# Kernel tuning notes

Hardware: AMD Instinct MI355X
Metric: run time of the kernel (lower is better)

Reference implementation:

```python
import jax, jax.numpy as jnp
import numpy as np
import math

C_S, C_Z, H, D, P_QK, P_V = 384, 128, 12, 16, 4, 8
B, L = 1, 512

def setup_inputs() -> dict:
    ks = jax.random.split(jax.random.key(0), 16)
    sc = lambda fan_in: 1.0 / math.sqrt(fan_in)
    return {
        's': jax.random.normal(ks[0], (B, L, C_S), jnp.float32),
        'z': jax.random.normal(ks[1], (B, L, L, C_Z), jnp.float32),
        'R': jax.random.normal(ks[2], (B, L, 3, 3), jnp.float32),
        't': jax.random.normal(ks[3], (B, L, 3), jnp.float32),
        'g_s': jnp.ones((C_S,), jnp.float32),
        'b_s': jnp.zeros((C_S,), jnp.float32),
        'g_z': jnp.ones((C_Z,), jnp.float32),
        'b_z': jnp.zeros((C_Z,), jnp.float32),
        'Wq': jax.random.normal(ks[4], (C_S, H * D), jnp.float32) * sc(C_S),
        'Wk': jax.random.normal(ks[5], (C_S, H * D), jnp.float32) * sc(C_S),
        'Wv': jax.random.normal(ks[6], (C_S, H * D), jnp.float32) * sc(C_S),
        'Wqp': jax.random.normal(ks[7], (C_S, H * P_QK * 3), jnp.float32) * sc(C_S),
        'Wkp': jax.random.normal(ks[8], (C_S, H * P_QK * 3), jnp.float32) * sc(C_S),
        'Wvp': jax.random.normal(ks[9], (C_S, H * P_V * 3), jnp.float32) * sc(C_S),
        'Wpb': jax.random.normal(ks[10], (C_Z, H), jnp.float32) * sc(C_Z),
        'pw': jax.random.normal(ks[11], (H,), jnp.float32) * 0.1,
        'Wo': jax.random.normal(ks[12], (H * D + H * P_V * 3 + H * P_V, C_S), jnp.float32) * sc(H * D + H * P_V * 3 + H * P_V),
        'bo': jnp.zeros((C_S,), jnp.float32),
    }

def _ln(x, g, b, eps=1e-5):
    mu = jnp.mean(x, axis=-1, keepdims=True)
    var = jnp.mean(jnp.square(x - mu), axis=-1, keepdims=True)
    return (x - mu) * jax.lax.rsqrt(var + eps) * g + b

def reference(s, z, R, t, g_s, b_s, g_z, b_z, Wq, Wk, Wv, Wqp, Wkp, Wvp, Wpb, pw, Wo, bo):
    Bn, Ln, _ = s.shape
    sn = _ln(s, g_s, b_s)
    zn = _ln(z, g_z, b_z)
    q_s = (sn @ Wq).reshape(Bn, Ln, H, D)
    k_s = (sn @ Wk).reshape(Bn, Ln, H, D)
    v_s = (sn @ Wv).reshape(Bn, Ln, H, D)
    q_pl = (sn @ Wqp).reshape(Bn, Ln, H, P_QK, 3)
    k_pl = (sn @ Wkp).reshape(Bn, Ln, H, P_QK, 3)
    v_pl = (sn @ Wvp).reshape(Bn, Ln, H, P_V, 3)
    # local->global frame transform: x_global = R x_local + t
    tb = t[:, :, None, None, :]
    q_p = jnp.einsum('blij,blhpj->blhpi', R, q_pl) + tb
    k_p = jnp.einsum('blij,blhpj->blhpi', R, k_pl) + tb
    v_p = jnp.einsum('blij,blhpj->blhpi', R, v_pl) + tb
    scalar_logits = jnp.einsum('bihd,bjhd->bijh', q_s, k_s) / math.sqrt(D)
    pair_logits = zn @ Wpb  # (B,L,L,H)
    # sum_p |q_ip - k_jp|^2 without materializing the (B,L,L,H,P,3) diff tensor
    qn2 = jnp.sum(jnp.square(q_p), axis=(-1, -2))  # (B,L,H)
    kn2 = jnp.sum(jnp.square(k_p), axis=(-1, -2))
    qk = jnp.einsum('bihpc,bjhpc->bijh', q_p, k_p)
    dist2 = qn2[:, :, None, :] + kn2[:, None, :, :] - 2.0 * qk
    w = jax.nn.softplus(pw)[None, None, None, :]
    logits = scalar_logits + pair_logits - 0.5 * w * dist2
    attn = jax.nn.softmax(logits, axis=2)  # over keys j
    out_s = jnp.einsum('bijh,bjhd->bihd', attn, v_s)
    out_pg = jnp.einsum('bijh,bjhpc->bihpc', attn, v_p)
    # global->local: R^T (x - t); (R^T)_{xy} = R_{yx}
    out_pl = jnp.einsum('blyx,blhpy->blhpx', R, out_pg - tb)
    out_pn = jnp.sqrt(jnp.sum(jnp.square(out_pl), axis=-1) + 1e-8)
    out_cat = jnp.concatenate([out_s.reshape(Bn, Ln, -1), out_pl.reshape(Bn, Ln, -1), out_pn.reshape(Bn, Ln, -1)], axis=-1)
    return s + out_cat @ Wo + bo
```

## Files before the change

### kernel.cpp

```cpp
#include <hip/hip_runtime.h>

typedef float f32x4 __attribute__((ext_vector_type(4)));
typedef short bf16x8 __attribute__((ext_vector_type(8)));

#define MFMA16(a,b,c) __builtin_amdgcn_mfma_f32_16x16x32_bf16((a),(b),(c),0,0,0)

__device__ __forceinline__ unsigned short f2bf(float f){
  unsigned int u = __builtin_bit_cast(unsigned int, f);
  u += 0x7FFFu + ((u>>16)&1u);
  return (unsigned short)(u>>16);
}

#define OFF_SNBF  0u
#define OFF_PROJ  393216u
#define OFF_QP    2752512u
#define OFF_KFRAG 3047424u
#define OFF_VFRAG 3440640u
#define OFF_KN2   4030464u
#define OFF_PLT   4055040u
#define OFF_OBUF  16637952u
#define OFF_CATBF 17620992u
#define OFF_WPBF  18210816u
#define OFF_GZF   18214912u
#define OFF_BZF   18223104u
#define OFF_WCF   18231296u
#define OFF_WOF   19116032u
#define OFF_WBUF  19558400u

__global__ __launch_bounds__(256) void k_prep(
    const float* __restrict__ Wq, const float* __restrict__ Wk, const float* __restrict__ Wv,
    const float* __restrict__ Wqp, const float* __restrict__ Wkp, const float* __restrict__ Wvp,
    const float* __restrict__ Wpb, const float* __restrict__ pw, const float* __restrict__ Wo,
    const float* __restrict__ g_z, const float* __restrict__ b_z,
    unsigned short* __restrict__ wpbfrag, float* __restrict__ gzfrag, float* __restrict__ bzfrag,
    unsigned short* __restrict__ wcfrag, unsigned short* __restrict__ wofrag,
    float* __restrict__ wbuf){
  int idx = blockIdx.x*256 + threadIdx.x;
  const int N_wpb = 2048, N_gz = 2048, N_wc = 72*12*64*8, N_wo = 24*18*64*8;
  if (idx < N_wpb){
    int r = idx&7, lane=(idx>>3)&63, chunk=idx>>9;
    int c = chunk*32 + ((lane>>4)<<3) + r; int h = lane&15;
    wpbfrag[idx] = (h<12) ? f2bf(Wpb[c*12+h]) : (unsigned short)0;
    return;
  }
  idx -= N_wpb;
  if (idx < N_gz){
    int r = idx&7, lane=(idx>>3)&63, chunk=idx>>9;
    int c = chunk*32 + ((lane>>4)<<3) + r;
    gzfrag[idx] = g_z[c]; bzfrag[idx] = b_z[c];
    return;
  }
  idx -= N_gz;
  if (idx < N_wc){
    int r = idx&7, lane=(idx>>3)&63, kt=(idx>>9)%12, nt=idx/(12*512);
    int k = kt*32 + ((lane>>4)<<3) + r; int n = nt*16 + (lane&15);
    float v;
    if      (n < 192) v = Wq [k*192 + n];
    else if (n < 384) v = Wk [k*192 + (n-192)];
    else if (n < 576) v = Wv [k*192 + (n-384)];
    else if (n < 720) v = Wqp[k*144 + (n-576)];
    else if (n < 864) v = Wkp[k*144 + (n-720)];
    else              v = Wvp[k*288 + (n-864)];
    wcfrag[idx] = f2bf(v);
    return;
  }
  idx -= N_wc;
  if (idx < N_wo){
    int r = idx&7, lane=(idx>>3)&63, kt=(idx>>9)%18, nt=idx/(18*512);
    int k = kt*32 + ((lane>>4)<<3) + r; int n = nt*16 + (lane&15);
    wofrag[idx] = f2bf(Wo[k*384 + n]);
    return;
  }
  idx -= N_wo;
  if (idx < 12){
    float x = pw[idx];
    wbuf[idx] = log1pf(expf(x));
  }
}

__global__ __launch_bounds__(64) void k_lns(const float* __restrict__ s,
    const float* __restrict__ g_s, const float* __restrict__ b_s,
    unsigned short* __restrict__ snbf){
  int l = blockIdx.x; int lane = threadIdx.x;
  float v[6]; float sum=0.f, ss=0.f;
  #pragma unroll
  for (int k=0;k<6;k++){
    float x = s[l*384 + lane + 64*k];
    v[k]=x; sum += x; ss = fmaf(x,x,ss);
  }
  #pragma unroll
  for (int m=1;m<64;m<<=1){ sum += __shfl_xor(sum,m); ss += __shfl_xor(ss,m); }
  float mu = sum*(1.f/384.f);
  float var = ss*(1.f/384.f) - mu*mu;
  float rs = rsqrtf(var + 1e-5f);
  #pragma unroll
  for (int k=0;k<6;k++){
    int c = lane + 64*k;
    snbf[l*384 + c] = f2bf((v[k]-mu)*rs*g_s[c] + b_s[c]);
  }
}

__global__ __launch_bounds__(256) void k_proj(const unsigned short* __restrict__ snbf,
    const unsigned short* __restrict__ wcfrag, float* __restrict__ proj){
  int wid = blockIdx.x*4 + (threadIdx.x>>6);
  int lane = threadIdx.x & 63;
  int il = lane&15, ig = lane>>4;
  int nt = wid % 72, ib = wid / 72;
  int i0 = ib*16;
  f32x4 acc = {0.f,0.f,0.f,0.f};
  #pragma unroll
  for (int kt=0; kt<12; kt++){
    bf16x8 a = *(const bf16x8*)(snbf + (i0+il)*384 + kt*32 + ig*8);
    bf16x8 b = *(const bf16x8*)(wcfrag + (size_t)((nt*12+kt)*64 + lane)*8);
    acc = MFMA16(a, b, acc);
  }
  #pragma unroll
  for (int r=0;r<4;r++)
    proj[(i0 + ig*4 + r)*1152 + nt*16 + il] = acc[r];
}

__global__ __launch_bounds__(192) void k_points(const float* __restrict__ proj,
    const float* __restrict__ Rm, const float* __restrict__ tv,
    float* __restrict__ qpb, unsigned short* __restrict__ kfrag,
    unsigned short* __restrict__ vfrag, float* __restrict__ kn2T){
  int l = blockIdx.x; int t = threadIdx.x;
  __shared__ float Rl[9], tl[3];
  __shared__ float kp_lds[12][12];
  __shared__ float vp_lds[12][24];
  __shared__ float kn2acc[12][4];
  if (t < 9) Rl[t] = Rm[l*9 + t];
  if (t < 3) tl[t] = tv[l*3 + t];
  __syncthreads();
  int h = t >> 4, pt = t & 15;
  {
    int ptype = (pt<4)? 0 : ((pt<8)? 1 : 2);
    int p = pt - ((ptype==0)?0:((ptype==1)?4:8));
    int col0 = (ptype==0)?576:((ptype==1)?720:864);
    int stride = (ptype==2)?24:12;
    const float* src = proj + l*1152 + col0 + h*stride + p*3;
    float lx=src[0], ly=src[1], lz=src[2];
    float cx = Rl[0]*lx + Rl[1]*ly + Rl[2]*lz + tl[0];
    float cy = Rl[3]*lx + Rl[4]*ly + Rl[5]*lz + tl[1];
    float cz = Rl[6]*lx + Rl[7]*ly + Rl[8]*lz + tl[2];
    if (ptype==0){
      float* d = qpb + (l*12 + h)*12 + p*3;
      d[0]=cx; d[1]=cy; d[2]=cz;
    } else if (ptype==1){
      kp_lds[h][p*3+0]=cx; kp_lds[h][p*3+1]=cy; kp_lds[h][p*3+2]=cz;
      kn2acc[h][p] = cx*cx + cy*cy + cz*cz;
    } else {
      vp_lds[h][p*3+0]=cx; vp_lds[h][p*3+1]=cy; vp_lds[h][p*3+2]=cz;
    }
  }
  __syncthreads();
  if (t < 12)
    kn2T[t*512 + l] = kn2acc[t][0]+kn2acc[t][1]+kn2acc[t][2]+kn2acc[t][3];
  {
    int jt = l >> 4, jl = l & 15;
    int q = pt >> 2, rr = (pt & 3)*2;
    unsigned short* dst = kfrag + (size_t)((h*32 + jt)*64 + 16*q + jl)*8 + rr;
    #pragma unroll
    for (int e=0;e<2;e++){
      int k = pt*2 + e; float f;
      if (k < 16)      f = proj[l*1152 + 192 + h*16 + k];
      else if (k < 28) f = kp_lds[h][k-16];
      else             f = 0.f;
      dst[e] = f2bf(f);
    }
  }
  {
    int d = pt; int jc = l >> 5; int jin = l & 31;
    int qq = (jin & 15) >> 2;
    int rr = (jin & 3) + ((jin >> 4) << 2);
    #pragma unroll
    for (int dt=0; dt<3; dt++){
      int dd = dt*16 + d; float f;
      if (dd < 16)      f = proj[l*1152 + 384 + h*16 + dd];
      else if (dd < 40) f = vp_lds[h][dd-16];
      else              f = 0.f;
      vfrag[(size_t)(((h*16 + jc)*3 + dt)*64 + 16*qq + d)*8 + rr] = f2bf(f);
    }
  }
}

__global__ __launch_bounds__(256) void k_pairbias(const float* __restrict__ z,
    const unsigned short* __restrict__ wpbfrag, const float* __restrict__ gzfrag,
    const float* __restrict__ bzfrag, const float* __restrict__ kn2T,
    const float* __restrict__ wbuf, float* __restrict__ plT){
  int w = blockIdx.x*4 + (threadIdx.x>>6);
  int lane = threadIdx.x & 63;
  int il = lane & 15, ig = lane >> 4;
  int nw = gridDim.x*4;
  f32x4 gzv[8], bzv[8];
  bf16x8 wf[4];
  #pragma unroll
  for (int c=0;c<4;c++){
    gzv[2*c]   = *(const f32x4*)(gzfrag + (c*64+lane)*8);
    gzv[2*c+1] = *(const f32x4*)(gzfrag + (c*64+lane)*8 + 4);
    bzv[2*c]   = *(const f32x4*)(bzfrag + (c*64+lane)*8);
    bzv[2*c+1] = *(const f32x4*)(bzfrag + (c*64+lane)*8 + 4);
    wf[c] = *(const bf16x8*)(wpbfrag + (c*64+lane)*8);
  }
  float wneg = (il<12) ? -0.5f*wbuf[il] : 0.f;
  for (int g = w; g < 16384; g += nw){
    int j = g >> 5; int i0 = (g & 31) << 4;
    const float* zr = z + (size_t)((i0+il)*512 + j)*128;
    f32x4 zv[8];
    #pragma unroll
    for (int c=0;c<4;c++){
      zv[2*c]   = *(const f32x4*)(zr + c*32 + ig*8);
      zv[2*c+1] = *(const f32x4*)(zr + c*32 + ig*8 + 4);
    }
    float sum=0.f, ss=0.f;
    #pragma unroll
    for (int m=0;m<8;m++)
      #pragma unroll
      for (int e=0;e<4;e++){ float x = zv[m][e]; sum += x; ss = fmaf(x,x,ss); }
    sum += __shfl_xor(sum,16); sum += __shfl_xor(sum,32);
    ss  += __shfl_xor(ss,16);  ss  += __shfl_xor(ss,32);
    float mu  = sum*(1.f/128.f);
    float var = ss*(1.f/128.f) - mu*mu;
    float rs  = rsqrtf(var + 1e-5f);
    f32x4 acc = {0.f,0.f,0.f,0.f};
    #pragma unroll
    for (int c=0;c<4;c++){
      bf16x8 zf;
      #pragma unroll
      for (int r=0;r<8;r++){
        float gv = (r<4)? gzv[2*c][r&3] : gzv[2*c+1][r&3];
        float bv = (r<4)? bzv[2*c][r&3] : bzv[2*c+1][r&3];
        float xv = (r<4)? zv[2*c][r&3]  : zv[2*c+1][r&3];
        zf[r] = (short)f2bf((xv-mu)*(rs*gv) + bv);
      }
      acc = MFMA16(zf, wf[c], acc);
    }
    if (il < 12){
      float tadd = wneg * kn2T[il*512 + j];
      f32x4 ov;
      ov[0]=acc[0]+tadd; ov[1]=acc[1]+tadd; ov[2]=acc[2]+tadd; ov[3]=acc[3]+tadd;
      *(f32x4*)(plT + (size_t)(il*512 + j)*512 + i0 + ig*4) = ov;
    }
  }
}

__global__ __launch_bounds__(64) void k_attn(const float* __restrict__ proj,
    const float* __restrict__ qpb, const float* __restrict__ wbuf,
    const unsigned short* __restrict__ kfrag, const float* __restrict__ plT,
    const unsigned short* __restrict__ vfrag, float* __restrict__ obuf){
  int u = blockIdx.x;
  int h = u % 12, ib = u / 12;
  int i0 = ib*16;
  int lane = threadIdx.x;
  int il = lane & 15, ig = lane >> 4;
  float wh = wbuf[h];
  bf16x8 qfrag;
  #pragma unroll
  for (int r=0;r<8;r++){
    int k = ig*8 + r; float f;
    if (k < 16)      f = proj[(i0+il)*1152 + h*16 + k]*0.25f;
    else if (k < 28) f = qpb[((i0+il)*12 + h)*12 + (k-16)]*wh;
    else             f = 0.f;
    qfrag[r] = (short)f2bf(f);
  }
  f32x4 sv[32];
  const unsigned short* kbase = kfrag + (size_t)(h*32)*64*8;
  #pragma unroll
  for (int jt=0;jt<32;jt++){
    bf16x8 kf = *(const bf16x8*)(kbase + (size_t)(jt*64 + lane)*8);
    f32x4 c0;
    #pragma unroll
    for (int r=0;r<4;r++)
      c0[r] = plT[(size_t)(h*512 + jt*16 + ig*4 + r)*512 + i0 + il];
    sv[jt] = MFMA16(kf, qfrag, c0);
  }
  float mx = -3.0e38f;
  #pragma unroll
  for (int jt=0;jt<32;jt++){
    #pragma unroll
    for (int r=0;r<4;r++) mx = fmaxf(mx, sv[jt][r]);
  }
  mx = fmaxf(mx, __shfl_xor(mx,16));
  mx = fmaxf(mx, __shfl_xor(mx,32));
  float sum = 0.f;
  #pragma unroll
  for (int jt=0;jt<32;jt++){
    #pragma unroll
    for (int r=0;r<4;r++){ float p = __expf(sv[jt][r]-mx); sv[jt][r]=p; sum+=p; }
  }
  sum += __shfl_xor(sum,16);
  sum += __shfl_xor(sum,32);
  float rden = 1.f/sum;
  f32x4 o0={0.f,0.f,0.f,0.f}, o1=o0, o2=o0;
  const unsigned short* vbase = vfrag + (size_t)(h*16)*3*64*8;
  #pragma unroll
  for (int jc=0;jc<16;jc++){
    bf16x8 pfrag;
    #pragma unroll
    for (int r=0;r<8;r++) pfrag[r] = (short)f2bf(sv[2*jc + (r>>2)][r&3]);
    bf16x8 v0 = *(const bf16x8*)(vbase + (size_t)((jc*3+0)*64 + lane)*8);
    bf16x8 v1 = *(const bf16x8*)(vbase + (size_t)((jc*3+1)*64 + lane)*8);
    bf16x8 v2 = *(const bf16x8*)(vbase + (size_t)((jc*3+2)*64 + lane)*8);
    o0 = MFMA16(v0, pfrag, o0);
    o1 = MFMA16(v1, pfrag, o1);
    o2 = MFMA16(v2, pfrag, o2);
  }
  float* orow = obuf + (i0+il)*480 + h*40;
  #pragma unroll
  for (int r=0;r<4;r++){
    orow[ig*4 + r]      = o0[r]*rden;
    orow[16 + ig*4 + r] = o1[r]*rden;
    if (ig < 2) orow[32 + ig*4 + r] = o2[r]*rden;
  }
}

__global__ __launch_bounds__(192) void k_cat(const float* __restrict__ obuf,
    const float* __restrict__ Rm, const float* __restrict__ tv,
    unsigned short* __restrict__ catbf){
  int l = blockIdx.x; int t = threadIdx.x;
  __shared__ float Rl[9], tl[3];
  if (t < 9) Rl[t] = Rm[l*9 + t];
  if (t < 3) tl[t] = tv[l*3 + t];
  __syncthreads();
  catbf[l*576 + t] = f2bf(obuf[l*480 + (t>>4)*40 + (t&15)]);
  if (t < 96){
    int hh = t >> 3, p = t & 7;
    float oy0 = obuf[l*480 + hh*40 + 16 + p*3 + 0] - tl[0];
    float oy1 = obuf[l*480 + hh*40 + 16 + p*3 + 1] - tl[1];
    float oy2 = obuf[l*480 + hh*40 + 16 + p*3 + 2] - tl[2];
    float px = Rl[0]*oy0 + Rl[3]*oy1 + Rl[6]*oy2;
    float py = Rl[1]*oy0 + Rl[4]*oy1 + Rl[7]*oy2;
    float pz = Rl[2]*oy0 + Rl[5]*oy1 + Rl[8]*oy2;
    catbf[l*576 + 192 + t*3 + 0] = f2bf(px);
    catbf[l*576 + 192 + t*3 + 1] = f2bf(py);
    catbf[l*576 + 192 + t*3 + 2] = f2bf(pz);
    catbf[l*576 + 480 + t] = f2bf(sqrtf(px*px + py*py + pz*pz + 1e-8f));
  }
}

__global__ __launch_bounds__(256) void k_outgemm(const unsigned short* __restrict__ catbf,
    const unsigned short* __restrict__ wofrag, const float* __restrict__ s,
    const float* __restrict__ bo, float* __restrict__ out){
  int wid = blockIdx.x*4 + (threadIdx.x>>6);
  int lane = threadIdx.x & 63;
  int il = lane&15, ig = lane>>4;
  int nt = wid % 24, ib = wid / 24;
  int i0 = ib*16;
  int n = nt*16 + il;
  f32x4 acc = {0.f,0.f,0.f,0.f};
  #pragma unroll
  for (int kt=0; kt<18; kt++){
    bf16x8 a = *(const bf16x8*)(catbf + (i0+il)*576 + kt*32 + ig*8);
    bf16x8 b = *(const bf16x8*)(wofrag + (size_t)((nt*18+kt)*64 + lane)*8);
    acc = MFMA16(a, b, acc);
  }
  float bv = bo[n];
  #pragma unroll
  for (int r=0;r<4;r++){
    int row = i0 + ig*4 + r;
    out[row*384 + n] = s[row*384 + n] + bv + acc[r];
  }
}

extern "C" void kernel_launch(void* const* d_in, const int* in_sizes, int n_in,
                              void* d_out, int out_size, void* d_ws, size_t ws_size,
                              hipStream_t stream) {
  const float* s   = (const float*)d_in[0];
  const float* z   = (const float*)d_in[1];
  const float* R   = (const float*)d_in[2];
  const float* t   = (const float*)d_in[3];
  const float* g_s = (const float*)d_in[4];
  const float* b_s = (const float*)d_in[5];
  const float* g_z = (const float*)d_in[6];
  const float* b_z = (const float*)d_in[7];
  const float* Wq  = (const float*)d_in[8];
  const float* Wk  = (const float*)d_in[9];
  const float* Wv  = (const float*)d_in[10];
  const float* Wqp = (const float*)d_in[11];
  const float* Wkp = (const float*)d_in[12];
  const float* Wvp = (const float*)d_in[13];
  const float* Wpb = (const float*)d_in[14];
  const float* pw  = (const float*)d_in[15];
  const float* Wo  = (const float*)d_in[16];
  const float* bo  = (const float*)d_in[17];
  float* out = (float*)d_out;
  char* ws = (char*)d_ws;

  unsigned short* snbf    = (unsigned short*)(ws + OFF_SNBF);
  float*          proj    = (float*)(ws + OFF_PROJ);
  float*          qpb     = (float*)(ws + OFF_QP);
  unsigned short* kfrag   = (unsigned short*)(ws + OFF_KFRAG);
  unsigned short* vfrag   = (unsigned short*)(ws + OFF_VFRAG);
  float*          kn2T    = (float*)(ws + OFF_KN2);
  float*          plT     = (float*)(ws + OFF_PLT);
  float*          obuf    = (float*)(ws + OFF_OBUF);
  unsigned short* catbf   = (unsigned short*)(ws + OFF_CATBF);
  unsigned short* wpbfrag = (unsigned short*)(ws + OFF_WPBF);
  float*          gzfrag  = (float*)(ws + OFF_GZF);
  float*          bzfrag  = (float*)(ws + OFF_BZF);
  unsigned short* wcfrag  = (unsigned short*)(ws + OFF_WCF);
  unsigned short* wofrag  = (unsigned short*)(ws + OFF_WOF);
  float*          wbuf    = (float*)(ws + OFF_WBUF);

  k_prep<<<2609, 256, 0, stream>>>(Wq, Wk, Wv, Wqp, Wkp, Wvp, Wpb, pw, Wo, g_z, b_z,
                                   wpbfrag, gzfrag, bzfrag, wcfrag, wofrag, wbuf);
  k_lns<<<512, 64, 0, stream>>>(s, g_s, b_s, snbf);
  k_proj<<<576, 256, 0, stream>>>(snbf, wcfrag, proj);
  k_points<<<512, 192, 0, stream>>>(proj, R, t, qpb, kfrag, vfrag, kn2T);
  k_pairbias<<<1024, 256, 0, stream>>>(z, wpbfrag, gzfrag, bzfrag, kn2T, wbuf, plT);
  k_attn<<<384, 64, 0, stream>>>(proj, qpb, wbuf, kfrag, plT, vfrag, obuf);
  k_cat<<<512, 192, 0, stream>>>(obuf, R, t, catbf);
  k_outgemm<<<192, 256, 0, stream>>>(catbf, wofrag, s, bo, out);
}
```

Measured before the change: 71.17 us.

## Store pair bias in bf16, split attention keys across 8 waves, fold LN into prep

The pair-bias intermediate is now written as bf16 instead of fp32, which halves its write and read traffic. The kn2 distance term moves out of k_pairbias and into the attention kernel. k_attn now runs 512 threads per block, with each of 8 waves handling 64 keys and combining its softmax max, sum and output partials through LDS. The LayerNorm of s is merged into the prep kernel to save one launch. In exchange the pair logits lose precision, and the attention kernel gains barriers and LDS reductions.

```diff
diff --git a/kernel.cpp b/kernel.cpp
--- a/kernel.cpp
+++ b/kernel.cpp
@@ -2,6 +2,7 @@
 
 typedef float f32x4 __attribute__((ext_vector_type(4)));
 typedef short bf16x8 __attribute__((ext_vector_type(8)));
+typedef unsigned short u16x4 __attribute__((ext_vector_type(4)));
 
 #define MFMA16(a,b,c) __builtin_amdgcn_mfma_f32_16x16x32_bf16((a),(b),(c),0,0,0)
 
@@ -9,6 +10,9 @@
   unsigned int u = __builtin_bit_cast(unsigned int, f);
   u += 0x7FFFu + ((u>>16)&1u);
   return (unsigned short)(u>>16);
+}
+__device__ __forceinline__ float bf2f(unsigned short u){
+  return __builtin_bit_cast(float, ((unsigned int)u)<<16);
 }
 
 #define OFF_SNBF  0u
@@ -18,16 +22,18 @@
 #define OFF_VFRAG 3440640u
 #define OFF_KN2   4030464u
 #define OFF_PLT   4055040u
-#define OFF_OBUF  16637952u
-#define OFF_CATBF 17620992u
-#define OFF_WPBF  18210816u
-#define OFF_GZF   18214912u
-#define OFF_BZF   18223104u
-#define OFF_WCF   18231296u
-#define OFF_WOF   19116032u
-#define OFF_WBUF  19558400u
+#define OFF_OBUF  10346496u
+#define OFF_CATBF 11329536u
+#define OFF_WPBF  11919360u
+#define OFF_GZF   11923456u
+#define OFF_BZF   11931648u
+#define OFF_WCF   11939840u
+#define OFF_WOF   12824576u
+#define OFF_WBUF  13266944u
 
 __global__ __launch_bounds__(256) void k_prep(
+    const float* __restrict__ s, const float* __restrict__ g_s, const float* __restrict__ b_s,
+    unsigned short* __restrict__ snbf,
     const float* __restrict__ Wq, const float* __restrict__ Wk, const float* __restrict__ Wv,
     const float* __restrict__ Wqp, const float* __restrict__ Wkp, const float* __restrict__ Wvp,
     const float* __restrict__ Wpb, const float* __restrict__ pw, const float* __restrict__ Wo,
@@ -35,7 +41,28 @@
     unsigned short* __restrict__ wpbfrag, float* __restrict__ gzfrag, float* __restrict__ bzfrag,
     unsigned short* __restrict__ wcfrag, unsigned short* __restrict__ wofrag,
     float* __restrict__ wbuf){
-  int idx = blockIdx.x*256 + threadIdx.x;
+  if (blockIdx.x < 128){
+    int l = blockIdx.x*4 + (threadIdx.x>>6);
+    int lane = threadIdx.x & 63;
+    float v[6]; float sum=0.f, ss=0.f;
+    #pragma unroll
+    for (int k=0;k<6;k++){
+      float x = s[l*384 + lane + 64*k];
+      v[k]=x; sum += x; ss = fmaf(x,x,ss);
+    }
+    #pragma unroll
+    for (int m=1;m<64;m<<=1){ sum += __shfl_xor(sum,m); ss += __shfl_xor(ss,m); }
+    float mu = sum*(1.f/384.f);
+    float var = ss*(1.f/384.f) - mu*mu;
+    float rs = rsqrtf(var + 1e-5f);
+    #pragma unroll
+    for (int k=0;k<6;k++){
+      int c = lane + 64*k;
+      snbf[l*384 + c] = f2bf((v[k]-mu)*rs*g_s[c] + b_s[c]);
+    }
+    return;
+  }
+  int idx = (blockIdx.x-128)*256 + threadIdx.x;
   const int N_wpb = 2048, N_gz = 2048, N_wc = 72*12*64*8, N_wo = 24*18*64*8;
   if (idx < N_wpb){
     int r = idx&7, lane=(idx>>3)&63, chunk=idx>>9;
@@ -75,28 +102,6 @@
   if (idx < 12){
     float x = pw[idx];
     wbuf[idx] = log1pf(expf(x));
-  }
-}
-
-__global__ __launch_bounds__(64) void k_lns(const float* __restrict__ s,
-    const float* __restrict__ g_s, const float* __restrict__ b_s,
-    unsigned short* __restrict__ snbf){
-  int l = blockIdx.x; int lane = threadIdx.x;
-  float v[6]; float sum=0.f, ss=0.f;
-  #pragma unroll
-  for (int k=0;k<6;k++){
-    float x = s[l*384 + lane + 64*k];
-    v[k]=x; sum += x; ss = fmaf(x,x,ss);
-  }
-  #pragma unroll
-  for (int m=1;m<64;m<<=1){ sum += __shfl_xor(sum,m); ss += __shfl_xor(ss,m); }
-  float mu = sum*(1.f/384.f);
-  float var = ss*(1.f/384.f) - mu*mu;
-  float rs = rsqrtf(var + 1e-5f);
-  #pragma unroll
-  for (int k=0;k<6;k++){
-    int c = lane + 64*k;
-    snbf[l*384 + c] = f2bf((v[k]-mu)*rs*g_s[c] + b_s[c]);
   }
 }
 
@@ -185,8 +190,7 @@
 
 __global__ __launch_bounds__(256) void k_pairbias(const float* __restrict__ z,
     const unsigned short* __restrict__ wpbfrag, const float* __restrict__ gzfrag,
-    const float* __restrict__ bzfrag, const float* __restrict__ kn2T,
-    const float* __restrict__ wbuf, float* __restrict__ plT){
+    const float* __restrict__ bzfrag, unsigned short* __restrict__ plTbf){
   int w = blockIdx.x*4 + (threadIdx.x>>6);
   int lane = threadIdx.x & 63;
   int il = lane & 15, ig = lane >> 4;
@@ -201,7 +205,6 @@
     bzv[2*c+1] = *(const f32x4*)(bzfrag + (c*64+lane)*8 + 4);
     wf[c] = *(const bf16x8*)(wpbfrag + (c*64+lane)*8);
   }
-  float wneg = (il<12) ? -0.5f*wbuf[il] : 0.f;
   for (int g = w; g < 16384; g += nw){
     int j = g >> 5; int i0 = (g & 31) << 4;
     const float* zr = z + (size_t)((i0+il)*512 + j)*128;
@@ -235,24 +238,30 @@
       acc = MFMA16(zf, wf[c], acc);
     }
     if (il < 12){
-      float tadd = wneg * kn2T[il*512 + j];
-      f32x4 ov;
-      ov[0]=acc[0]+tadd; ov[1]=acc[1]+tadd; ov[2]=acc[2]+tadd; ov[3]=acc[3]+tadd;
-      *(f32x4*)(plT + (size_t)(il*512 + j)*512 + i0 + ig*4) = ov;
-    }
-  }
-}
-
-__global__ __launch_bounds__(64) void k_attn(const float* __restrict__ proj,
+      u16x4 ov;
+      #pragma unroll
+      for (int r=0;r<4;r++) ov[r] = f2bf(acc[r]);
+      *(u16x4*)(plTbf + (size_t)(il*512 + j)*512 + i0 + ig*4) = ov;
+    }
+  }
+}
+
+__global__ __launch_bounds__(512) void k_attn(const float* __restrict__ proj,
     const float* __restrict__ qpb, const float* __restrict__ wbuf,
-    const unsigned short* __restrict__ kfrag, const float* __restrict__ plT,
-    const unsigned short* __restrict__ vfrag, float* __restrict__ obuf){
+    const unsigned short* __restrict__ kfrag, const unsigned short* __restrict__ plTbf,
+    const float* __restrict__ kn2T, const unsigned short* __restrict__ vfrag,
+    float* __restrict__ obuf){
   int u = blockIdx.x;
   int h = u % 12, ib = u / 12;
   int i0 = ib*16;
-  int lane = threadIdx.x;
+  int tid = threadIdx.x;
+  int w = tid >> 6, lane = tid & 63;
   int il = lane & 15, ig = lane >> 4;
+  __shared__ float red[8][16];
+  __shared__ float gsum[16];
+  __shared__ float osum[8][64][13];
   float wh = wbuf[h];
+  float wneg = -0.5f*wh;
   bf16x8 qfrag;
   #pragma unroll
   for (int r=0;r<8;r++){
@@ -262,41 +271,59 @@
     else             f = 0.f;
     qfrag[r] = (short)f2bf(f);
   }
-  f32x4 sv[32];
+  int jt0 = w*4;
+  f32x4 sv[4];
   const unsigned short* kbase = kfrag + (size_t)(h*32)*64*8;
-  #pragma unroll
-  for (int jt=0;jt<32;jt++){
+  const unsigned short* pbase = plTbf + (size_t)(h*512)*512;
+  const float* kbn = kn2T + h*512;
+  #pragma unroll
+  for (int jj=0;jj<4;jj++){
+    int jt = jt0+jj;
     bf16x8 kf = *(const bf16x8*)(kbase + (size_t)(jt*64 + lane)*8);
     f32x4 c0;
     #pragma unroll
-    for (int r=0;r<4;r++)
-      c0[r] = plT[(size_t)(h*512 + jt*16 + ig*4 + r)*512 + i0 + il];
-    sv[jt] = MFMA16(kf, qfrag, c0);
+    for (int r=0;r<4;r++){
+      int j = jt*16 + ig*4 + r;
+      c0[r] = bf2f(pbase[(size_t)j*512 + i0 + il]) + wneg*kbn[j];
+    }
+    sv[jj] = MFMA16(kf, qfrag, c0);
   }
   float mx = -3.0e38f;
   #pragma unroll
-  for (int jt=0;jt<32;jt++){
-    #pragma unroll
-    for (int r=0;r<4;r++) mx = fmaxf(mx, sv[jt][r]);
+  for (int jj=0;jj<4;jj++){
+    #pragma unroll
+    for (int r=0;r<4;r++) mx = fmaxf(mx, sv[jj][r]);
   }
   mx = fmaxf(mx, __shfl_xor(mx,16));
   mx = fmaxf(mx, __shfl_xor(mx,32));
+  if (lane < 16) red[w][lane] = mx;
+  __syncthreads();
+  float gm = red[0][il];
+  #pragma unroll
+  for (int ww=1;ww<8;ww++) gm = fmaxf(gm, red[ww][il]);
+  __syncthreads();
   float sum = 0.f;
   #pragma unroll
-  for (int jt=0;jt<32;jt++){
-    #pragma unroll
-    for (int r=0;r<4;r++){ float p = __expf(sv[jt][r]-mx); sv[jt][r]=p; sum+=p; }
+  for (int jj=0;jj<4;jj++){
+    #pragma unroll
+    for (int r=0;r<4;r++){ float p = __expf(sv[jj][r]-gm); sv[jj][r]=p; sum+=p; }
   }
   sum += __shfl_xor(sum,16);
   sum += __shfl_xor(sum,32);
-  float rden = 1.f/sum;
+  if (lane < 16) red[w][lane] = sum;
+  __syncthreads();
+  float gs = 0.f;
+  #pragma unroll
+  for (int ww=0;ww<8;ww++) gs += red[ww][il];
+  if (w == 0 && lane < 16) gsum[lane] = gs;
   f32x4 o0={0.f,0.f,0.f,0.f}, o1=o0, o2=o0;
   const unsigned short* vbase = vfrag + (size_t)(h*16)*3*64*8;
   #pragma unroll
-  for (int jc=0;jc<16;jc++){
+  for (int jcl=0;jcl<2;jcl++){
+    int jc = w*2 + jcl;
     bf16x8 pfrag;
     #pragma unroll
-    for (int r=0;r<8;r++) pfrag[r] = (short)f2bf(sv[2*jc + (r>>2)][r&3]);
+    for (int r=0;r<8;r++) pfrag[r] = (short)f2bf(sv[2*jcl + (r>>2)][r&3]);
     bf16x8 v0 = *(const bf16x8*)(vbase + (size_t)((jc*3+0)*64 + lane)*8);
     bf16x8 v1 = *(const bf16x8*)(vbase + (size_t)((jc*3+1)*64 + lane)*8);
     bf16x8 v2 = *(const bf16x8*)(vbase + (size_t)((jc*3+2)*64 + lane)*8);
@@ -304,12 +331,22 @@
     o1 = MFMA16(v1, pfrag, o1);
     o2 = MFMA16(v2, pfrag, o2);
   }
-  float* orow = obuf + (i0+il)*480 + h*40;
   #pragma unroll
   for (int r=0;r<4;r++){
-    orow[ig*4 + r]      = o0[r]*rden;
-    orow[16 + ig*4 + r] = o1[r]*rden;
-    if (ig < 2) orow[32 + ig*4 + r] = o2[r]*rden;
+    osum[w][lane][r]   = o0[r];
+    osum[w][lane][4+r] = o1[r];
+    osum[w][lane][8+r] = o2[r];
+  }
+  __syncthreads();
+  for (int idx = tid; idx < 640; idx += 512){
+    int i = idx & 15, d = idx >> 4;
+    int seg = d >> 4, dr = d & 15;
+    int lx = ((dr>>2) << 4) + i;
+    int c = seg*4 + (dr & 3);
+    float v = 0.f;
+    #pragma unroll
+    for (int ww=0;ww<8;ww++) v += osum[ww][lx][c];
+    obuf[(i0+i)*480 + h*40 + d] = v / gsum[i];
   }
 }
 
@@ -391,7 +428,7 @@
   unsigned short* kfrag   = (unsigned short*)(ws + OFF_KFRAG);
   unsigned short* vfrag   = (unsigned short*)(ws + OFF_VFRAG);
   float*          kn2T    = (float*)(ws + OFF_KN2);
-  float*          plT     = (float*)(ws + OFF_PLT);
+  unsigned short* plTbf   = (unsigned short*)(ws + OFF_PLT);
   float*          obuf    = (float*)(ws + OFF_OBUF);
   unsigned short* catbf   = (unsigned short*)(ws + OFF_CATBF);
   unsigned short* wpbfrag = (unsigned short*)(ws + OFF_WPBF);
@@ -401,13 +438,13 @@
   unsigned short* wofrag  = (unsigned short*)(ws + OFF_WOF);
   float*          wbuf    = (float*)(ws + OFF_WBUF);
 
-  k_prep<<<2609, 256, 0, stream>>>(Wq, Wk, Wv, Wqp, Wkp, Wvp, Wpb, pw, Wo, g_z, b_z,
+  k_prep<<<2737, 256, 0, stream>>>(s, g_s, b_s, snbf,
+                                   Wq, Wk, Wv, Wqp, Wkp, Wvp, Wpb, pw, Wo, g_z, b_z,
                                    wpbfrag, gzfrag, bzfrag, wcfrag, wofrag, wbuf);
-  k_lns<<<512, 64, 0, stream>>>(s, g_s, b_s, snbf);
   k_proj<<<576, 256, 0, stream>>>(snbf, wcfrag, proj);
   k_points<<<512, 192, 0, stream>>>(proj, R, t, qpb, kfrag, vfrag, kn2T);
-  k_pairbias<<<1024, 256, 0, stream>>>(z, wpbfrag, gzfrag, bzfrag, kn2T, wbuf, plT);
-  k_attn<<<384, 64, 0, stream>>>(proj, qpb, wbuf, kfrag, plT, vfrag, obuf);
+  k_pairbias<<<1024, 256, 0, stream>>>(z, wpbfrag, gzfrag, bzfrag, plTbf);
+  k_attn<<<384, 512, 0, stream>>>(proj, qpb, wbuf, kfrag, plTbf, kn2T, vfrag, obuf);
   k_cat<<<512, 192, 0, stream>>>(obuf, R, t, catbf);
   k_outgemm<<<192, 256, 0, stream>>>(catbf, wofrag, s, bo, out);
 }
```

After: 61.04 us. 14.2% less time.
